# Kernel optimization log

Measured on AMD Instinct MI355X. Metric: run time of the kernel, lower is better.

The kernel has to match this reference:

```python
import jax, jax.numpy as jnp
import numpy as np

SCORE_THR = 0.3   # SSD.score_threshold
NMS_THR = 0.6     # SSD.nms_threshold
TOP_K = 100       # fixed candidate count per class (jit-friendly padded NMS)
CODER_W = (10.0, 10.0, 5.0, 5.0)  # SSD.coder_weights
B, A, C = 32, 8732, 81


def setup_inputs() -> dict:
    key = jax.random.key(0)
    k1, k2, k3 = jax.random.split(key, 3)
    class_logits = jax.random.normal(k1, (B, A, C), jnp.float32)
    box_regression = jax.random.normal(k2, (B, A, 4), jnp.float32)
    u = jax.random.uniform(k3, (A, 4), jnp.float32)
    centers = u[:, :2]                      # cy, cx in [0,1]
    sizes = 0.05 + 0.45 * u[:, 2:]          # h, w in [0.05, 0.5]
    priors = jnp.concatenate([centers, sizes], axis=-1)  # [A,4] (cy,cx,h,w)
    return {"class_logits": class_logits, "box_regression": box_regression, "priors": priors}


def decode_boxes(rel, priors):
    # rel: [...,A,4] codes (ty,tx,th,tw); priors: [A,4] (cy,cx,h,w); standard TF SSD box coder
    ty = rel[..., 0] / CODER_W[0]
    tx = rel[..., 1] / CODER_W[1]
    th = rel[..., 2] / CODER_W[2]
    tw = rel[..., 3] / CODER_W[3]
    cy = ty * priors[..., 2] + priors[..., 0]
    cx = tx * priors[..., 3] + priors[..., 1]
    h = jnp.exp(th) * priors[..., 2]
    w = jnp.exp(tw) * priors[..., 3]
    # corners (ymin, xmin, ymax, xmax)
    return jnp.stack([cy - h / 2, cx - w / 2, cy + h / 2, cx + w / 2], axis=-1)


def _iou_matrix(b):
    # b: [K,4] corners -> [K,K] pairwise IoU
    area = jnp.clip(b[:, 2] - b[:, 0], 0) * jnp.clip(b[:, 3] - b[:, 1], 0)
    tl = jnp.maximum(b[:, None, :2], b[None, :, :2])
    br = jnp.minimum(b[:, None, 2:], b[None, :, 2:])
    wh = jnp.clip(br - tl, 0)
    inter = wh[..., 0] * wh[..., 1]
    return inter / (area[:, None] + area[None, :] - inter + 1e-9)


def _nms_one_class(boxes, probs):
    # boxes: [A,4], probs: [A] -> padded [TOP_K,5] (box + score, zeros where suppressed)
    valid_all = probs > SCORE_THR
    masked = jnp.where(valid_all, probs, -1.0)
    top, idx = jax.lax.top_k(masked, TOP_K)          # sorted descending
    b = boxes[idx]                                    # [TOP_K,4]
    valid = top > SCORE_THR
    iou = _iou_matrix(jax.lax.stop_gradient(b))       # NMS selection is non-differentiable
    rng = jnp.arange(TOP_K)

    def body(i, keep):
        cur = keep[i] & valid[i]
        sup = (iou[i] > NMS_THR) & (rng > i)
        return jnp.where(cur, keep & ~sup, keep)

    keep = jax.lax.fori_loop(0, TOP_K, body, jnp.ones((TOP_K,), bool)) & valid
    out_b = jnp.where(keep[:, None], b, 0.0)
    out_s = jnp.where(keep, top, 0.0)
    return jnp.concatenate([out_b, out_s[:, None]], axis=-1)  # [TOP_K,5]


def reference(class_logits, box_regression, priors):
    scores = jax.nn.sigmoid(class_logits)             # [B,A,C]
    boxes = decode_boxes(box_regression, priors)      # [B,A,4]
    fg = scores[..., 1:]                              # skip background class 0 -> [B,A,C-1]
    per_class = jax.vmap(_nms_one_class, in_axes=(None, 1))   # over classes
    per_image = jax.vmap(per_class, in_axes=(0, 0))           # over batch
    return per_image(boxes, fg)                       # [B, C-1, TOP_K, 5]
```

## Files before the change

kernel.cpp:

```cpp
#include <hip/hip_runtime.h>
#include <math.h>

#define A_N   8732
#define A_PAD 8736
#define C_N   81
#define B_N   32
#define NCLS  80
#define NTASK (B_N * NCLS)
#define TOPK  100
#define NTHR  256
#define CAND  512
#define TA    64
#define NV4K  (A_PAD / 8)
#define KPT16 5
#define K0    0xBE00u
#define NBIN  128

#define THR_LOGIT (-0.8472978603872034)

__device__ __forceinline__ unsigned mapf(float x) {
    unsigned b = __float_as_uint(x);
    return b ^ ((b & 0x80000000u) ? 0xFFFFFFFFu : 0x80000000u);
}
__device__ __forceinline__ float unmapf(unsigned u) {
    unsigned b = (u & 0x80000000u) ? (u ^ 0x80000000u) : ~u;
    return __uint_as_float(b);
}

__device__ __forceinline__ void dec64(const float4 r4, const float4 p4,
                                      double* bx, double* area) {
    double ty = (double)r4.x / 10.0, tx = (double)r4.y / 10.0;
    double th = (double)r4.z / 5.0,  tw = (double)r4.w / 5.0;
    double cy = ty * (double)p4.z + (double)p4.x;
    double cx = tx * (double)p4.w + (double)p4.y;
    double hh = exp(th) * (double)p4.z;
    double ww = exp(tw) * (double)p4.w;
    bx[0] = cy - hh / 2.0; bx[1] = cx - ww / 2.0;
    bx[2] = cy + hh / 2.0; bx[3] = cx + ww / 2.0;
    double e0 = bx[2] - bx[0]; if (e0 < 0.0) e0 = 0.0;
    double e1 = bx[3] - bx[1]; if (e1 < 0.0) e1 = 0.0;
    *area = e0 * e1;
}

__global__ __launch_bounds__(NTHR) void key_transpose_kernel(
    const float* __restrict__ logits,
    unsigned short* __restrict__ keys)
{
    __shared__ unsigned short tile[NCLS][TA + 2];
    const int NT = (A_N + TA - 1) / TA;
    const int b  = blockIdx.x / NT;
    const int t0 = blockIdx.x % NT;
    const int a0 = t0 * TA;
    const int an = min(TA, A_N - a0);
    const int tid = threadIdx.x;

    const float* src = logits + ((size_t)b * A_N + a0) * C_N;

    if (an == TA) {
        const float4* src4 = (const float4*)src;
        const int total4 = TA * C_N / 4;
        for (int i = tid; i < total4; i += NTHR) {
            float4 v = src4[i];
            int base = 4 * i;
            int r  = base / C_N;
            int ch = base - r * C_N;
            float xs[4] = { v.x, v.y, v.z, v.w };
            #pragma unroll
            for (int k = 0; k < 4; ++k) {
                if (ch > 0)
                    tile[ch - 1][r] = (unsigned short)
                        (((double)xs[k] > THR_LOGIT) ? (mapf(xs[k]) >> 16) : 0u);
                if (++ch == C_N) { ch = 0; ++r; }
            }
        }
        __syncthreads();
        for (int i = tid; i < NCLS * 8; i += NTHR) {
            int row = i >> 3, j = i & 7;
            const unsigned* t32 = (const unsigned*)&tile[row][8 * j];
            uint4 w;
            w.x = t32[0]; w.y = t32[1]; w.z = t32[2]; w.w = t32[3];
            *(uint4*)(keys + ((size_t)(b * NCLS + row)) * A_PAD + a0 + 8 * j) = w;
        }
    } else {
        const int total = an * C_N;
        for (int i = tid; i < total; i += NTHR) {
            int r = i / C_N, ch = i - r * C_N;
            float x = src[i];
            if (ch > 0)
                tile[ch - 1][r] = (unsigned short)
                    (((double)x > THR_LOGIT) ? (mapf(x) >> 16) : 0u);
        }
        __syncthreads();
        for (int i = tid; i < NCLS * TA; i += NTHR) {
            int row = i / TA, col = i - row * TA;
            int a = a0 + col;
            if (a < A_PAD)
                keys[((size_t)(b * NCLS + row)) * A_PAD + a] =
                    (col < an) ? tile[row][col] : (unsigned short)0;
        }
    }
}

__device__ __forceinline__ void hcount(unsigned k, unsigned* hist) {
    if (k >= K0) {
        unsigned bin = (k - K0) >> 4; if (bin > (NBIN - 1)) bin = NBIN - 1;
        atomicAdd(&hist[bin], 1u);
    }
}

__global__ __launch_bounds__(NTHR) void ssd_nms_kernel(
    const float* __restrict__ logits,
    const unsigned short* __restrict__ keys,
    const float* __restrict__ boxreg,
    const float* __restrict__ priors,
    float* __restrict__ out)
{
    const int task = blockIdx.x;
    const int b = task / NCLS;
    const int c = task % NCLS;
    const int tid = threadIdx.x;

    __shared__ unsigned hist[NBIN];
    __shared__ unsigned candi[CAND];
    __shared__ unsigned long long cand[CAND];
    __shared__ unsigned long long ssel[TOPK];
    __shared__ float fb0[TOPK], fb1[TOPK], fb2[TOPK], fb3[TOPK];
    __shared__ float farea[TOPK], fscore[TOPK];
    __shared__ float4 rbox[TOPK], pbox[TOPK];
    __shared__ int svalid[TOPK];
    __shared__ unsigned long long supmask[TOPK][2];
    __shared__ unsigned long long keepw[2];
    __shared__ unsigned wtot[2];
    __shared__ int scal[2];

    const float* lg = logits + ((size_t)b * A_N * C_N) + (c + 1);

    uint4 kreg[KPT16];
    {
        const uint4* ksrc = (const uint4*)(keys + (size_t)task * A_PAD);
        #pragma unroll
        for (int j = 0; j < KPT16; ++j) {
            int i = tid + j * NTHR;
            kreg[j] = (i < NV4K) ? ksrc[i] : make_uint4(0u, 0u, 0u, 0u);
        }
    }

    if (tid < NBIN) hist[tid] = 0;
    for (int i = tid; i < CAND; i += NTHR) cand[i] = 0ull;
    if (tid < TOPK) ssel[tid] = 0ull;
    if (tid == 0) { scal[0] = 0; scal[1] = 1; }
    __syncthreads();

    #pragma unroll
    for (int j = 0; j < KPT16; ++j) {
        uint4 v = kreg[j];
        hcount(v.x & 0xFFFFu, hist); hcount(v.x >> 16, hist);
        hcount(v.y & 0xFFFFu, hist); hcount(v.y >> 16, hist);
        hcount(v.z & 0xFFFFu, hist); hcount(v.z >> 16, hist);
        hcount(v.w & 0xFFFFu, hist); hcount(v.w >> 16, hist);
    }
    __syncthreads();

    {
        unsigned h = (tid < NBIN) ? hist[tid] : 0u;
        unsigned incl = h;
        int lane = tid & 63;
        #pragma unroll
        for (int off = 1; off < 64; off <<= 1) {
            unsigned v = __shfl_down(incl, off);
            if (lane + off < 64) incl += v;
        }
        if (tid < NBIN && lane == 0) wtot[tid >> 6] = incl;
        __syncthreads();
        if (tid < NBIN) {
            unsigned S = incl + ((tid < 64) ? wtot[1] : 0u);
            if (S >= TOPK && (S - h) < TOPK)
                scal[1] = (int)(K0 + ((unsigned)tid << 4));
        }
        __syncthreads();

        unsigned T = wtot[0] + wtot[1];
        if (T < TOPK) {
            if (tid < NBIN) hist[tid] = 0;
            __syncthreads();
            #pragma unroll
            for (int j = 0; j < KPT16; ++j) {
                uint4 v = kreg[j];
                unsigned k;
                k = v.x & 0xFFFFu; if (k >= 0x4000u && k < K0) atomicAdd(&hist[(k - 0x4000u) >> 8], 1u);
                k = v.x >> 16;     if (k >= 0x4000u && k < K0) atomicAdd(&hist[(k - 0x4000u) >> 8], 1u);
                k = v.y & 0xFFFFu; if (k >= 0x4000u && k < K0) atomicAdd(&hist[(k - 0x4000u) >> 8], 1u);
                k = v.y >> 16;     if (k >= 0x4000u && k < K0) atomicAdd(&hist[(k - 0x4000u) >> 8], 1u);
                k = v.z & 0xFFFFu; if (k >= 0x4000u && k < K0) atomicAdd(&hist[(k - 0x4000u) >> 8], 1u);
                k = v.z >> 16;     if (k >= 0x4000u && k < K0) atomicAdd(&hist[(k - 0x4000u) >> 8], 1u);
                k = v.w & 0xFFFFu; if (k >= 0x4000u && k < K0) atomicAdd(&hist[(k - 0x4000u) >> 8], 1u);
                k = v.w >> 16;     if (k >= 0x4000u && k < K0) atomicAdd(&hist[(k - 0x4000u) >> 8], 1u);
            }
            __syncthreads();
            unsigned h2 = (tid < NBIN) ? hist[tid] : 0u;
            unsigned incl2 = h2;
            #pragma unroll
            for (int off = 1; off < 64; off <<= 1) {
                unsigned v = __shfl_down(incl2, off);
                if (lane + off < 64) incl2 += v;
            }
            if (tid < NBIN && lane == 0) wtot[tid >> 6] = incl2;
            __syncthreads();
            if (tid < NBIN) {
                unsigned S2 = incl2 + ((tid < 64) ? wtot[1] : 0u);
                unsigned need = TOPK - T;
                if (S2 >= need && (S2 - h2) < need)
                    scal[1] = (int)(0x4000u + ((unsigned)tid << 8));
            }
            __syncthreads();
        }
    }
    const unsigned cut16 = (unsigned)scal[1];

    #pragma unroll
    for (int j = 0; j < KPT16; ++j) {
        uint4 v = kreg[j];
        int a8 = 8 * (tid + j * NTHR);
        unsigned k; int p;
        k = v.x & 0xFFFFu; if (k >= cut16) { p = atomicAdd(&scal[0],1); if (p<CAND) candi[p] = a8+0; }
        k = v.x >> 16;     if (k >= cut16) { p = atomicAdd(&scal[0],1); if (p<CAND) candi[p] = a8+1; }
        k = v.y & 0xFFFFu; if (k >= cut16) { p = atomicAdd(&scal[0],1); if (p<CAND) candi[p] = a8+2; }
        k = v.y >> 16;     if (k >= cut16) { p = atomicAdd(&scal[0],1); if (p<CAND) candi[p] = a8+3; }
        k = v.z & 0xFFFFu; if (k >= cut16) { p = atomicAdd(&scal[0],1); if (p<CAND) candi[p] = a8+4; }
        k = v.z >> 16;     if (k >= cut16) { p = atomicAdd(&scal[0],1); if (p<CAND) candi[p] = a8+5; }
        k = v.w & 0xFFFFu; if (k >= cut16) { p = atomicAdd(&scal[0],1); if (p<CAND) candi[p] = a8+6; }
        k = v.w >> 16;     if (k >= cut16) { p = atomicAdd(&scal[0],1); if (p<CAND) candi[p] = a8+7; }
    }
    __syncthreads();
    const int M = min(scal[0], CAND);

    for (int i = tid; i < M; i += NTHR) {
        unsigned a = candi[i];
        float x = lg[(size_t)a * C_N];
        cand[i] = ((unsigned long long)mapf(x) << 32) | (unsigned)(~a);
    }
    __syncthreads();

    {
        int Mr = (M + 7) & ~7;
        for (int i = tid; i < Mr; i += NTHR) {
            unsigned long long mykey = cand[i];
            int rank = 0;
            #pragma unroll 8
            for (int j = 0; j < Mr; ++j) rank += (cand[j] > mykey) ? 1 : 0;
            if (mykey != 0ull && rank < TOPK) ssel[rank] = mykey;
        }
    }
    __syncthreads();

    if (tid < TOPK) {
        unsigned long long key = ssel[tid];
        int valid = (key != 0ull);
        float b0 = 0, b1 = 0, b2 = 0, b3 = 0, area = 0, sc = 0;
        float4 r4 = make_float4(0.f, 0.f, 0.f, 0.f), p4 = r4;
        if (valid) {
            int a = (int)(~(unsigned)key);
            float x = unmapf((unsigned)(key >> 32));
            sc = 1.0f / (1.0f + __expf(-x));
            r4 = *(const float4*)(boxreg + ((size_t)b * A_N + a) * 4);
            p4 = *(const float4*)(priors + (size_t)a * 4);
            float ty = r4.x * 0.1f, tx = r4.y * 0.1f;
            float th = r4.z * 0.2f, tw = r4.w * 0.2f;
            float cy = ty * p4.z + p4.x;
            float cx = tx * p4.w + p4.y;
            float hh = __expf(th) * p4.z;
            float ww = __expf(tw) * p4.w;
            b0 = cy - hh * 0.5f; b1 = cx - ww * 0.5f;
            b2 = cy + hh * 0.5f; b3 = cx + ww * 0.5f;
            area = fmaxf(b2 - b0, 0.f) * fmaxf(b3 - b1, 0.f);
        }
        fb0[tid] = b0; fb1[tid] = b1; fb2[tid] = b2; fb3[tid] = b3;
        farea[tid] = area; fscore[tid] = sc;
        rbox[tid] = r4; pbox[tid] = p4;
        svalid[tid] = valid;
    }
    __syncthreads();

    if (tid < 2 * TOPK) {
        int i = tid >> 1, w = tid & 1;
        unsigned long long m = 0;
        if (svalid[i]) {
            float i0 = fb0[i], i1 = fb1[i], i2 = fb2[i], i3 = fb3[i], ia = farea[i];
            int jbase = w * 64;
            int jend = min(jbase + 64, TOPK);
            int jstart = (jbase > i + 1) ? jbase : (i + 1);
            for (int j = jstart; j < jend; ++j) {
                float tl0 = fmaxf(i0, fb0[j]);
                float tl1 = fmaxf(i1, fb1[j]);
                float br0 = fminf(i2, fb2[j]);
                float br1 = fminf(i3, fb3[j]);
                float wh0 = fmaxf(br0 - tl0, 0.0f);
                float wh1 = fmaxf(br1 - tl1, 0.0f);
                float inter = wh0 * wh1;
                float denom = (ia + farea[j]) - inter;
                bool sup = inter > 0.601f * denom;
                bool amb = !sup && (inter > 0.599f * denom) && (inter > 0.0f);
                if (__any(amb)) {
                    if (amb) {
                        double bi[4], bj[4], ai, aj;
                        dec64(rbox[i], pbox[i], bi, &ai);
                        dec64(rbox[j], pbox[j], bj, &aj);
                        double tl0d = fmax(bi[0], bj[0]);
                        double tl1d = fmax(bi[1], bj[1]);
                        double br0d = fmin(bi[2], bj[2]);
                        double br1d = fmin(bi[3], bj[3]);
                        double wh0d = br0d - tl0d; if (wh0d < 0.0) wh0d = 0.0;
                        double wh1d = br1d - tl1d; if (wh1d < 0.0) wh1d = 0.0;
                        double interd = wh0d * wh1d;
                        double denomd = ((ai + aj) - interd) + 1e-9;
                        sup = interd > 0.6 * denomd;
                    }
                }
                if (sup) m |= 1ull << (j - jbase);
            }
        }
        supmask[i][w] = m;
    }
    __syncthreads();

    if (tid == 0) {
        unsigned long long kp0 = ~0ull, kp1 = ~0ull;
        for (int i = 0; i < TOPK; ++i) {
            bool kb = (i < 64) ? ((kp0 >> i) & 1ull) : ((kp1 >> (i - 64)) & 1ull);
            if (kb && svalid[i]) { kp0 &= ~supmask[i][0]; kp1 &= ~supmask[i][1]; }
        }
        keepw[0] = kp0; keepw[1] = kp1;
    }
    __syncthreads();

    if (tid < TOPK) {
        bool kb = (tid < 64) ? ((keepw[0] >> tid) & 1ull)
                             : ((keepw[1] >> (tid - 64)) & 1ull);
        bool kp = kb && (svalid[tid] != 0);
        size_t base = ((size_t)task * TOPK + tid) * 5;
        out[base + 0] = kp ? fb0[tid] : 0.0f;
        out[base + 1] = kp ? fb1[tid] : 0.0f;
        out[base + 2] = kp ? fb2[tid] : 0.0f;
        out[base + 3] = kp ? fb3[tid] : 0.0f;
        out[base + 4] = kp ? fscore[tid] : 0.0f;
    }
}

__global__ __launch_bounds__(NTHR) void ssd_nms_fallback(
    const float* __restrict__ logits,
    const float* __restrict__ boxreg,
    const float* __restrict__ priors,
    float* __restrict__ out)
{
    const int task = blockIdx.x;
    const int b = task / NCLS;
    const int c = task % NCLS;
    const int tid = threadIdx.x;

    __shared__ unsigned hist[2048];
    __shared__ unsigned wt4[4];
    __shared__ unsigned candi[CAND];
    __shared__ unsigned long long cand[CAND];
    __shared__ unsigned long long ssel[TOPK];
    __shared__ float fb0[TOPK], fb1[TOPK], fb2[TOPK], fb3[TOPK];
    __shared__ float farea[TOPK], fscore[TOPK];
    __shared__ float4 rbox[TOPK], pbox[TOPK];
    __shared__ int svalid[TOPK];
    __shared__ unsigned long long supmask[TOPK][2];
    __shared__ unsigned long long keepw[2];
    __shared__ int scal[2];

    const float* lg = logits + ((size_t)b * A_N * C_N) + (c + 1);

    for (int k = tid; k < 2048; k += NTHR) hist[k] = 0;
    for (int i = tid; i < CAND; i += NTHR) cand[i] = 0ull;
    if (tid < TOPK) ssel[tid] = 0ull;
    if (tid == 0) { scal[0] = 0; scal[1] = 1; }
    __syncthreads();

    for (int a = tid; a < A_N; a += NTHR) {
        float x = lg[(size_t)a * C_N];
        if ((double)x > THR_LOGIT) atomicAdd(&hist[mapf(x) >> 21], 1u);
    }
    __syncthreads();
    {
        unsigned s = 0;
        #pragma unroll
        for (int k = 0; k < 8; ++k) s += hist[tid * 8 + k];
        unsigned incl = s;
        int lane = tid & 63;
        #pragma unroll
        for (int off = 1; off < 64; off <<= 1) {
            unsigned v = __shfl_down(incl, off);
            if (lane + off < 64) incl += v;
        }
        if (lane == 0) wt4[tid >> 6] = incl;
        __syncthreads();
        unsigned hi = 0;
        #pragma unroll
        for (int w = 0; w < 4; ++w) if (w > (tid >> 6)) hi += wt4[w];
        unsigned excl = hi + (incl - s);
        if (excl < TOPK && excl + s >= TOPK) {
            unsigned running = excl;
            #pragma unroll
            for (int k = 7; k >= 0; --k) {
                running += hist[tid * 8 + k];
                if (running >= TOPK) { scal[1] = (int)(((unsigned)(tid * 8 + k)) << 21); break; }
            }
        }
    }
    __syncthreads();
    const unsigned cutoff = (unsigned)scal[1];

    for (int a = tid; a < A_N; a += NTHR) {
        float x = lg[(size_t)a * C_N];
        if ((double)x > THR_LOGIT) {
            unsigned u = mapf(x);
            if (u >= cutoff) {
                int p = atomicAdd(&scal[0], 1);
                if (p < CAND) { candi[p] = (unsigned)a; cand[p] = ((unsigned long long)u << 32) | (unsigned)(~(unsigned)a); }
            }
        }
    }
    __syncthreads();
    const int M = min(scal[0], CAND);
    {
        int Mr = (M + 7) & ~7;
        for (int i = tid; i < Mr; i += NTHR) {
            unsigned long long mykey = cand[i];
            int rank = 0;
            for (int j = 0; j < Mr; ++j) rank += (cand[j] > mykey) ? 1 : 0;
            if (mykey != 0ull && rank < TOPK) ssel[rank] = mykey;
        }
    }
    __syncthreads();
    if (tid < TOPK) {
        unsigned long long key = ssel[tid];
        int valid = (key != 0ull);
        float b0 = 0, b1 = 0, b2 = 0, b3 = 0, area = 0, sc = 0;
        float4 r4 = make_float4(0.f,0.f,0.f,0.f), p4 = r4;
        if (valid) {
            int a = (int)(~(unsigned)key);
            float x = unmapf((unsigned)(key >> 32));
            sc = 1.0f / (1.0f + __expf(-x));
            r4 = *(const float4*)(boxreg + ((size_t)b * A_N + a) * 4);
            p4 = *(const float4*)(priors + (size_t)a * 4);
            float cy = r4.x * 0.1f * p4.z + p4.x;
            float cx = r4.y * 0.1f * p4.w + p4.y;
            float hh = __expf(r4.z * 0.2f) * p4.z;
            float ww = __expf(r4.w * 0.2f) * p4.w;
            b0 = cy - hh * 0.5f; b1 = cx - ww * 0.5f;
            b2 = cy + hh * 0.5f; b3 = cx + ww * 0.5f;
            area = fmaxf(b2 - b0, 0.f) * fmaxf(b3 - b1, 0.f);
        }
        fb0[tid]=b0; fb1[tid]=b1; fb2[tid]=b2; fb3[tid]=b3;
        farea[tid]=area; fscore[tid]=sc; rbox[tid]=r4; pbox[tid]=p4; svalid[tid]=valid;
    }
    __syncthreads();
    if (tid < 2 * TOPK) {
        int i = tid >> 1, w = tid & 1;
        unsigned long long m = 0;
        if (svalid[i]) {
            float i0=fb0[i], i1=fb1[i], i2=fb2[i], i3=fb3[i], ia=farea[i];
            int jbase = w * 64, jend = min(jbase + 64, TOPK);
            int jstart = (jbase > i + 1) ? jbase : (i + 1);
            for (int j = jstart; j < jend; ++j) {
                float tl0=fmaxf(i0,fb0[j]), tl1=fmaxf(i1,fb1[j]);
                float br0=fminf(i2,fb2[j]), br1=fminf(i3,fb3[j]);
                float wh0=fmaxf(br0-tl0,0.f), wh1=fmaxf(br1-tl1,0.f);
                float inter=wh0*wh1, denom=(ia+farea[j])-inter;
                bool sup = inter > 0.601f*denom;
                bool amb = !sup && (inter > 0.599f*denom) && (inter > 0.f);
                if (__any(amb)) {
                    if (amb) {
                        double bi[4], bj[4], ai, aj;
                        dec64(rbox[i], pbox[i], bi, &ai);
                        dec64(rbox[j], pbox[j], bj, &aj);
                        double wh0d = fmin(bi[2],bj[2]) - fmax(bi[0],bj[0]); if (wh0d<0) wh0d=0;
                        double wh1d = fmin(bi[3],bj[3]) - fmax(bi[1],bj[1]); if (wh1d<0) wh1d=0;
                        double interd = wh0d*wh1d;
                        sup = interd > 0.6 * (((ai+aj)-interd)+1e-9);
                    }
                }
                if (sup) m |= 1ull << (j - jbase);
            }
        }
        supmask[i][w] = m;
    }
    __syncthreads();
    if (tid == 0) {
        unsigned long long kp0 = ~0ull, kp1 = ~0ull;
        for (int i = 0; i < TOPK; ++i) {
            bool kb = (i < 64) ? ((kp0 >> i) & 1ull) : ((kp1 >> (i - 64)) & 1ull);
            if (kb && svalid[i]) { kp0 &= ~supmask[i][0]; kp1 &= ~supmask[i][1]; }
        }
        keepw[0] = kp0; keepw[1] = kp1;
    }
    __syncthreads();
    if (tid < TOPK) {
        bool kb = (tid < 64) ? ((keepw[0] >> tid) & 1ull)
                             : ((keepw[1] >> (tid - 64)) & 1ull);
        bool kp = kb && (svalid[tid] != 0);
        size_t base = ((size_t)task * TOPK + tid) * 5;
        out[base + 0] = kp ? fb0[tid] : 0.0f;
        out[base + 1] = kp ? fb1[tid] : 0.0f;
        out[base + 2] = kp ? fb2[tid] : 0.0f;
        out[base + 3] = kp ? fb3[tid] : 0.0f;
        out[base + 4] = kp ? fscore[tid] : 0.0f;
    }
}

extern "C" void kernel_launch(void* const* d_in, const int* in_sizes, int n_in,
                              void* d_out, int out_size, void* d_ws, size_t ws_size,
                              hipStream_t stream) {
    const float* logits = (const float*)d_in[0];
    const float* boxreg = (const float*)d_in[1];
    const float* priors = (const float*)d_in[2];
    float* out = (float*)d_out;

    const size_t keys_bytes = (size_t)NTASK * A_PAD * sizeof(unsigned short);
    if (ws_size >= keys_bytes) {
        unsigned short* keysw = (unsigned short*)d_ws;
        const int NT = (A_N + TA - 1) / TA;
        key_transpose_kernel<<<dim3(B_N * NT), dim3(NTHR), 0, stream>>>(logits, keysw);
        ssd_nms_kernel<<<dim3(NTASK), dim3(NTHR), 0, stream>>>(
            logits, keysw, boxreg, priors, out);
    } else {
        ssd_nms_fallback<<<dim3(NTASK), dim3(NTHR), 0, stream>>>(
            logits, boxreg, priors, out);
    }
}
```

Before: 97.95 us.

## Rewrite per-class NMS kernel as single-wavefront block without barriers

The NMS kernel now runs one 64-lane wavefront per (image,class) task instead of a 256-thread block. Histogram scans, cutoff selection, candidate compaction and the keep-mask loop use wave shuffles and ballots, so no __syncthreads or shared atomics on counters are needed. The IoU mask work is split so lanes handle rows i and 99-i for load balance. Candidate capacity drops to 384 and keys are re-read from global memory rather than held in registers. Each block now has a quarter of the threads, so less parallelism per task is traded for no barrier overhead.

```diff
diff --git a/kernel.cpp b/kernel.cpp
--- a/kernel.cpp
+++ b/kernel.cpp
@@ -9,13 +9,12 @@
 #define NTASK (B_N * NCLS)
 #define TOPK  100
 #define NTHR  256
-#define CAND  512
+#define WAVE  64
+#define CAND  384
 #define TA    64
 #define NV4K  (A_PAD / 8)
-#define KPT16 5
+#define KPTW  18
 #define K0    0xBE00u
-#define NBIN  128
-
 #define THR_LOGIT (-0.8472978603872034)
 
 __device__ __forceinline__ unsigned mapf(float x) {
@@ -101,14 +100,7 @@
     }
 }
 
-__device__ __forceinline__ void hcount(unsigned k, unsigned* hist) {
-    if (k >= K0) {
-        unsigned bin = (k - K0) >> 4; if (bin > (NBIN - 1)) bin = NBIN - 1;
-        atomicAdd(&hist[bin], 1u);
-    }
-}
-
-__global__ __launch_bounds__(NTHR) void ssd_nms_kernel(
+__global__ __launch_bounds__(WAVE) void ssd_nms_wave(
     const float* __restrict__ logits,
     const unsigned short* __restrict__ keys,
     const float* __restrict__ boxreg,
@@ -118,231 +110,265 @@
     const int task = blockIdx.x;
     const int b = task / NCLS;
     const int c = task % NCLS;
-    const int tid = threadIdx.x;
-
-    __shared__ unsigned hist[NBIN];
+    const int l = threadIdx.x;
+
+    __shared__ unsigned hist[128];
     __shared__ unsigned candi[CAND];
     __shared__ unsigned long long cand[CAND];
     __shared__ unsigned long long ssel[TOPK];
-    __shared__ float fb0[TOPK], fb1[TOPK], fb2[TOPK], fb3[TOPK];
-    __shared__ float farea[TOPK], fscore[TOPK];
-    __shared__ float4 rbox[TOPK], pbox[TOPK];
-    __shared__ int svalid[TOPK];
-    __shared__ unsigned long long supmask[TOPK][2];
-    __shared__ unsigned long long keepw[2];
-    __shared__ unsigned wtot[2];
-    __shared__ int scal[2];
+    __shared__ float4 fbox4[TOPK];
+    __shared__ float farea[TOPK];
+    __shared__ int sanchor[TOPK];
 
     const float* lg = logits + ((size_t)b * A_N * C_N) + (c + 1);
-
-    uint4 kreg[KPT16];
+    const uint4* ksrc = (const uint4*)(keys + (size_t)task * A_PAD);
+    const float4* breg4 = (const float4*)(boxreg + (size_t)b * A_N * 4);
+    const float4* pri4  = (const float4*)priors;
+
+    hist[l] = 0; hist[WAVE + l] = 0;
+    ssel[l] = 0ull;
+    if (l < TOPK - WAVE) ssel[WAVE + l] = 0ull;
+
+    for (int j = 0; j < KPTW; ++j) {
+        int i = l + j * WAVE;
+        if (i < NV4K) {
+            uint4 v = ksrc[i];
+            unsigned k;
+            k = v.x & 0xFFFFu; if (k >= K0) { unsigned bn = (k - K0) >> 4; if (bn > 127u) bn = 127u; atomicAdd(&hist[bn], 1u); }
+            k = v.x >> 16;     if (k >= K0) { unsigned bn = (k - K0) >> 4; if (bn > 127u) bn = 127u; atomicAdd(&hist[bn], 1u); }
+            k = v.y & 0xFFFFu; if (k >= K0) { unsigned bn = (k - K0) >> 4; if (bn > 127u) bn = 127u; atomicAdd(&hist[bn], 1u); }
+            k = v.y >> 16;     if (k >= K0) { unsigned bn = (k - K0) >> 4; if (bn > 127u) bn = 127u; atomicAdd(&hist[bn], 1u); }
+            k = v.z & 0xFFFFu; if (k >= K0) { unsigned bn = (k - K0) >> 4; if (bn > 127u) bn = 127u; atomicAdd(&hist[bn], 1u); }
+            k = v.z >> 16;     if (k >= K0) { unsigned bn = (k - K0) >> 4; if (bn > 127u) bn = 127u; atomicAdd(&hist[bn], 1u); }
+            k = v.w & 0xFFFFu; if (k >= K0) { unsigned bn = (k - K0) >> 4; if (bn > 127u) bn = 127u; atomicAdd(&hist[bn], 1u); }
+            k = v.w >> 16;     if (k >= K0) { unsigned bn = (k - K0) >> 4; if (bn > 127u) bn = 127u; atomicAdd(&hist[bn], 1u); }
+        }
+    }
+
+    unsigned cut16 = 1u;
     {
-        const uint4* ksrc = (const uint4*)(keys + (size_t)task * A_PAD);
-        #pragma unroll
-        for (int j = 0; j < KPT16; ++j) {
-            int i = tid + j * NTHR;
-            kreg[j] = (i < NV4K) ? ksrc[i] : make_uint4(0u, 0u, 0u, 0u);
-        }
-    }
-
-    if (tid < NBIN) hist[tid] = 0;
-    for (int i = tid; i < CAND; i += NTHR) cand[i] = 0ull;
-    if (tid < TOPK) ssel[tid] = 0ull;
-    if (tid == 0) { scal[0] = 0; scal[1] = 1; }
-    __syncthreads();
-
-    #pragma unroll
-    for (int j = 0; j < KPT16; ++j) {
-        uint4 v = kreg[j];
-        hcount(v.x & 0xFFFFu, hist); hcount(v.x >> 16, hist);
-        hcount(v.y & 0xFFFFu, hist); hcount(v.y >> 16, hist);
-        hcount(v.z & 0xFFFFu, hist); hcount(v.z >> 16, hist);
-        hcount(v.w & 0xFFFFu, hist); hcount(v.w >> 16, hist);
-    }
-    __syncthreads();
-
-    {
-        unsigned h = (tid < NBIN) ? hist[tid] : 0u;
-        unsigned incl = h;
-        int lane = tid & 63;
+        unsigned sL = hist[l], sH = hist[WAVE + l];
+        unsigned inclH = sH, inclL = sL;
         #pragma unroll
         for (int off = 1; off < 64; off <<= 1) {
-            unsigned v = __shfl_down(incl, off);
-            if (lane + off < 64) incl += v;
-        }
-        if (tid < NBIN && lane == 0) wtot[tid >> 6] = incl;
-        __syncthreads();
-        if (tid < NBIN) {
-            unsigned S = incl + ((tid < 64) ? wtot[1] : 0u);
-            if (S >= TOPK && (S - h) < TOPK)
-                scal[1] = (int)(K0 + ((unsigned)tid << 4));
-        }
-        __syncthreads();
-
-        unsigned T = wtot[0] + wtot[1];
-        if (T < TOPK) {
-            if (tid < NBIN) hist[tid] = 0;
-            __syncthreads();
-            #pragma unroll
-            for (int j = 0; j < KPT16; ++j) {
-                uint4 v = kreg[j];
-                unsigned k;
-                k = v.x & 0xFFFFu; if (k >= 0x4000u && k < K0) atomicAdd(&hist[(k - 0x4000u) >> 8], 1u);
-                k = v.x >> 16;     if (k >= 0x4000u && k < K0) atomicAdd(&hist[(k - 0x4000u) >> 8], 1u);
-                k = v.y & 0xFFFFu; if (k >= 0x4000u && k < K0) atomicAdd(&hist[(k - 0x4000u) >> 8], 1u);
-                k = v.y >> 16;     if (k >= 0x4000u && k < K0) atomicAdd(&hist[(k - 0x4000u) >> 8], 1u);
-                k = v.z & 0xFFFFu; if (k >= 0x4000u && k < K0) atomicAdd(&hist[(k - 0x4000u) >> 8], 1u);
-                k = v.z >> 16;     if (k >= 0x4000u && k < K0) atomicAdd(&hist[(k - 0x4000u) >> 8], 1u);
-                k = v.w & 0xFFFFu; if (k >= 0x4000u && k < K0) atomicAdd(&hist[(k - 0x4000u) >> 8], 1u);
-                k = v.w >> 16;     if (k >= 0x4000u && k < K0) atomicAdd(&hist[(k - 0x4000u) >> 8], 1u);
-            }
-            __syncthreads();
-            unsigned h2 = (tid < NBIN) ? hist[tid] : 0u;
-            unsigned incl2 = h2;
+            unsigned t = __shfl_down(inclH, off); if (l + off < 64) inclH += t;
+        }
+        #pragma unroll
+        for (int off = 1; off < 64; off <<= 1) {
+            unsigned t = __shfl_down(inclL, off); if (l + off < 64) inclL += t;
+        }
+        unsigned TH = __shfl(inclH, 0);
+        unsigned SH = inclH;
+        unsigned SL = inclL + TH;
+        unsigned T  = __shfl(SL, 0);
+
+        if (T >= TOPK) {
+            bool crH = (SH >= TOPK) && (SH - sH < TOPK);
+            bool crL = (SL >= TOPK) && (SL - sL < TOPK);
+            unsigned myCut = crH ? (K0 + ((unsigned)(WAVE + l) << 4))
+                                 : (K0 + ((unsigned)l << 4));
+            unsigned long long cm = __ballot(crH || crL);
+            cut16 = __shfl(myCut, (int)(__ffsll((long long)cm) - 1));
+        } else {
+            hist[l] = 0; hist[WAVE + l] = 0;
+            for (int j = 0; j < KPTW; ++j) {
+                int i = l + j * WAVE;
+                if (i < NV4K) {
+                    uint4 v = ksrc[i];
+                    unsigned k;
+                    k = v.x & 0xFFFFu; if (k >= 0x4000u && k < K0) atomicAdd(&hist[(k - 0x4000u) >> 8], 1u);
+                    k = v.x >> 16;     if (k >= 0x4000u && k < K0) atomicAdd(&hist[(k - 0x4000u) >> 8], 1u);
+                    k = v.y & 0xFFFFu; if (k >= 0x4000u && k < K0) atomicAdd(&hist[(k - 0x4000u) >> 8], 1u);
+                    k = v.y >> 16;     if (k >= 0x4000u && k < K0) atomicAdd(&hist[(k - 0x4000u) >> 8], 1u);
+                    k = v.z & 0xFFFFu; if (k >= 0x4000u && k < K0) atomicAdd(&hist[(k - 0x4000u) >> 8], 1u);
+                    k = v.z >> 16;     if (k >= 0x4000u && k < K0) atomicAdd(&hist[(k - 0x4000u) >> 8], 1u);
+                    k = v.w & 0xFFFFu; if (k >= 0x4000u && k < K0) atomicAdd(&hist[(k - 0x4000u) >> 8], 1u);
+                    k = v.w >> 16;     if (k >= 0x4000u && k < K0) atomicAdd(&hist[(k - 0x4000u) >> 8], 1u);
+                }
+            }
+            unsigned sL2 = hist[l], sH2 = hist[WAVE + l];
+            unsigned iH = sH2, iL = sL2;
             #pragma unroll
             for (int off = 1; off < 64; off <<= 1) {
-                unsigned v = __shfl_down(incl2, off);
-                if (lane + off < 64) incl2 += v;
-            }
-            if (tid < NBIN && lane == 0) wtot[tid >> 6] = incl2;
-            __syncthreads();
-            if (tid < NBIN) {
-                unsigned S2 = incl2 + ((tid < 64) ? wtot[1] : 0u);
-                unsigned need = TOPK - T;
-                if (S2 >= need && (S2 - h2) < need)
-                    scal[1] = (int)(0x4000u + ((unsigned)tid << 8));
-            }
-            __syncthreads();
-        }
-    }
-    const unsigned cut16 = (unsigned)scal[1];
+                unsigned t = __shfl_down(iH, off); if (l + off < 64) iH += t;
+            }
+            #pragma unroll
+            for (int off = 1; off < 64; off <<= 1) {
+                unsigned t = __shfl_down(iL, off); if (l + off < 64) iL += t;
+            }
+            unsigned TH2 = __shfl(iH, 0);
+            unsigned SH2 = iH, SL2 = iL + TH2;
+            unsigned need = TOPK - T;
+            bool crH = (SH2 >= need) && (SH2 - sH2 < need);
+            bool crL = (SL2 >= need) && (SL2 - sL2 < need);
+            unsigned myCut = crH ? (0x4000u + ((unsigned)(WAVE + l) << 8))
+                                 : (0x4000u + ((unsigned)l << 8));
+            unsigned long long cm = __ballot(crH || crL);
+            if (cm) cut16 = __shfl(myCut, (int)(__ffsll((long long)cm) - 1));
+        }
+    }
+
+    int cnt = 0;
+    auto gstep = [&](unsigned kk, int idx) {
+        bool pr = (kk >= cut16);
+        unsigned long long mk = __ballot(pr);
+        if (pr) {
+            int pos = cnt + (int)__popcll(mk & ((1ull << l) - 1ull));
+            if (pos < CAND) candi[pos] = (unsigned)idx;
+        }
+        cnt += (int)__popcll(mk);
+    };
+    for (int j = 0; j < KPTW; ++j) {
+        int i = l + j * WAVE;
+        uint4 v = (i < NV4K) ? ksrc[i] : make_uint4(0u, 0u, 0u, 0u);
+        int a8 = 8 * i;
+        gstep(v.x & 0xFFFFu, a8 + 0); gstep(v.x >> 16, a8 + 1);
+        gstep(v.y & 0xFFFFu, a8 + 2); gstep(v.y >> 16, a8 + 3);
+        gstep(v.z & 0xFFFFu, a8 + 4); gstep(v.z >> 16, a8 + 5);
+        gstep(v.w & 0xFFFFu, a8 + 6); gstep(v.w >> 16, a8 + 7);
+    }
+    const int M  = min(cnt, CAND);
+    const int Mr = (M + 7) & ~7;
+    if (l < Mr - M) cand[M + l] = 0ull;
 
     #pragma unroll
-    for (int j = 0; j < KPT16; ++j) {
-        uint4 v = kreg[j];
-        int a8 = 8 * (tid + j * NTHR);
-        unsigned k; int p;
-        k = v.x & 0xFFFFu; if (k >= cut16) { p = atomicAdd(&scal[0],1); if (p<CAND) candi[p] = a8+0; }
-        k = v.x >> 16;     if (k >= cut16) { p = atomicAdd(&scal[0],1); if (p<CAND) candi[p] = a8+1; }
-        k = v.y & 0xFFFFu; if (k >= cut16) { p = atomicAdd(&scal[0],1); if (p<CAND) candi[p] = a8+2; }
-        k = v.y >> 16;     if (k >= cut16) { p = atomicAdd(&scal[0],1); if (p<CAND) candi[p] = a8+3; }
-        k = v.z & 0xFFFFu; if (k >= cut16) { p = atomicAdd(&scal[0],1); if (p<CAND) candi[p] = a8+4; }
-        k = v.z >> 16;     if (k >= cut16) { p = atomicAdd(&scal[0],1); if (p<CAND) candi[p] = a8+5; }
-        k = v.w & 0xFFFFu; if (k >= cut16) { p = atomicAdd(&scal[0],1); if (p<CAND) candi[p] = a8+6; }
-        k = v.w >> 16;     if (k >= cut16) { p = atomicAdd(&scal[0],1); if (p<CAND) candi[p] = a8+7; }
-    }
-    __syncthreads();
-    const int M = min(scal[0], CAND);
-
-    for (int i = tid; i < M; i += NTHR) {
-        unsigned a = candi[i];
-        float x = lg[(size_t)a * C_N];
-        cand[i] = ((unsigned long long)mapf(x) << 32) | (unsigned)(~a);
-    }
-    __syncthreads();
+    for (int k = 0; k < CAND / WAVE; ++k) {
+        int i = l + k * WAVE;
+        if (i < M) {
+            unsigned a = candi[i];
+            float x = lg[(size_t)a * C_N];
+            cand[i] = ((unsigned long long)mapf(x) << 32) | (unsigned)(~a);
+        }
+    }
 
     {
-        int Mr = (M + 7) & ~7;
-        for (int i = tid; i < Mr; i += NTHR) {
-            unsigned long long mykey = cand[i];
-            int rank = 0;
-            #pragma unroll 8
-            for (int j = 0; j < Mr; ++j) rank += (cand[j] > mykey) ? 1 : 0;
-            if (mykey != 0ull && rank < TOPK) ssel[rank] = mykey;
-        }
-    }
-    __syncthreads();
-
-    if (tid < TOPK) {
-        unsigned long long key = ssel[tid];
-        int valid = (key != 0ull);
-        float b0 = 0, b1 = 0, b2 = 0, b3 = 0, area = 0, sc = 0;
-        float4 r4 = make_float4(0.f, 0.f, 0.f, 0.f), p4 = r4;
-        if (valid) {
-            int a = (int)(~(unsigned)key);
-            float x = unmapf((unsigned)(key >> 32));
-            sc = 1.0f / (1.0f + __expf(-x));
-            r4 = *(const float4*)(boxreg + ((size_t)b * A_N + a) * 4);
-            p4 = *(const float4*)(priors + (size_t)a * 4);
-            float ty = r4.x * 0.1f, tx = r4.y * 0.1f;
-            float th = r4.z * 0.2f, tw = r4.w * 0.2f;
-            float cy = ty * p4.z + p4.x;
-            float cx = tx * p4.w + p4.y;
-            float hh = __expf(th) * p4.z;
-            float ww = __expf(tw) * p4.w;
-            b0 = cy - hh * 0.5f; b1 = cx - ww * 0.5f;
-            b2 = cy + hh * 0.5f; b3 = cx + ww * 0.5f;
-            area = fmaxf(b2 - b0, 0.f) * fmaxf(b3 - b1, 0.f);
-        }
-        fb0[tid] = b0; fb1[tid] = b1; fb2[tid] = b2; fb3[tid] = b3;
-        farea[tid] = area; fscore[tid] = sc;
-        rbox[tid] = r4; pbox[tid] = p4;
-        svalid[tid] = valid;
-    }
-    __syncthreads();
-
-    if (tid < 2 * TOPK) {
-        int i = tid >> 1, w = tid & 1;
-        unsigned long long m = 0;
-        if (svalid[i]) {
-            float i0 = fb0[i], i1 = fb1[i], i2 = fb2[i], i3 = fb3[i], ia = farea[i];
-            int jbase = w * 64;
-            int jend = min(jbase + 64, TOPK);
-            int jstart = (jbase > i + 1) ? jbase : (i + 1);
-            for (int j = jstart; j < jend; ++j) {
-                float tl0 = fmaxf(i0, fb0[j]);
-                float tl1 = fmaxf(i1, fb1[j]);
-                float br0 = fminf(i2, fb2[j]);
-                float br1 = fminf(i3, fb3[j]);
-                float wh0 = fmaxf(br0 - tl0, 0.0f);
-                float wh1 = fmaxf(br1 - tl1, 0.0f);
-                float inter = wh0 * wh1;
-                float denom = (ia + farea[j]) - inter;
-                bool sup = inter > 0.601f * denom;
-                bool amb = !sup && (inter > 0.599f * denom) && (inter > 0.0f);
-                if (__any(amb)) {
-                    if (amb) {
-                        double bi[4], bj[4], ai, aj;
-                        dec64(rbox[i], pbox[i], bi, &ai);
-                        dec64(rbox[j], pbox[j], bj, &aj);
-                        double tl0d = fmax(bi[0], bj[0]);
-                        double tl1d = fmax(bi[1], bj[1]);
-                        double br0d = fmin(bi[2], bj[2]);
-                        double br1d = fmin(bi[3], bj[3]);
-                        double wh0d = br0d - tl0d; if (wh0d < 0.0) wh0d = 0.0;
-                        double wh1d = br1d - tl1d; if (wh1d < 0.0) wh1d = 0.0;
-                        double interd = wh0d * wh1d;
-                        double denomd = ((ai + aj) - interd) + 1e-9;
-                        sup = interd > 0.6 * denomd;
-                    }
-                }
-                if (sup) m |= 1ull << (j - jbase);
-            }
-        }
-        supmask[i][w] = m;
-    }
-    __syncthreads();
-
-    if (tid == 0) {
-        unsigned long long kp0 = ~0ull, kp1 = ~0ull;
-        for (int i = 0; i < TOPK; ++i) {
-            bool kb = (i < 64) ? ((kp0 >> i) & 1ull) : ((kp1 >> (i - 64)) & 1ull);
-            if (kb && svalid[i]) { kp0 &= ~supmask[i][0]; kp1 &= ~supmask[i][1]; }
-        }
-        keepw[0] = kp0; keepw[1] = kp1;
-    }
-    __syncthreads();
-
-    if (tid < TOPK) {
-        bool kb = (tid < 64) ? ((keepw[0] >> tid) & 1ull)
-                             : ((keepw[1] >> (tid - 64)) & 1ull);
-        bool kp = kb && (svalid[tid] != 0);
-        size_t base = ((size_t)task * TOPK + tid) * 5;
-        out[base + 0] = kp ? fb0[tid] : 0.0f;
-        out[base + 1] = kp ? fb1[tid] : 0.0f;
-        out[base + 2] = kp ? fb2[tid] : 0.0f;
-        out[base + 3] = kp ? fb3[tid] : 0.0f;
-        out[base + 4] = kp ? fscore[tid] : 0.0f;
+        unsigned long long mk2[CAND / WAVE];
+        int rk[CAND / WAVE];
+        #pragma unroll
+        for (int k = 0; k < CAND / WAVE; ++k) {
+            int i = l + k * WAVE;
+            mk2[k] = (i < Mr) ? cand[i] : 0ull;
+            rk[k] = 0;
+        }
+        for (int j = 0; j < Mr; ++j) {
+            unsigned long long cj = cand[j];
+            #pragma unroll
+            for (int k = 0; k < CAND / WAVE; ++k)
+                if (k * WAVE < Mr)
+                    rk[k] += (cj > mk2[k]) ? 1 : 0;
+        }
+        #pragma unroll
+        for (int k = 0; k < CAND / WAVE; ++k)
+            if (mk2[k] != 0ull && rk[k] < TOPK) ssel[rk[k]] = mk2[k];
+    }
+
+    unsigned long long keyA = ssel[l];
+    unsigned long long keyB = (l < TOPK - WAVE) ? ssel[WAVE + l] : 0ull;
+    float A0 = 0, A1 = 0, A2 = 0, A3 = 0, arA = 0, scA = 0; int aA = 0;
+    float B0 = 0, B1 = 0, B2 = 0, B3 = 0, arB = 0, scB = 0; int aB = 0;
+    if (keyA) {
+        aA = (int)(~(unsigned)keyA);
+        float x = unmapf((unsigned)(keyA >> 32));
+        scA = 1.0f / (1.0f + __expf(-x));
+        float4 r4 = breg4[aA], p4 = pri4[aA];
+        float cy = r4.x * 0.1f * p4.z + p4.x;
+        float cx = r4.y * 0.1f * p4.w + p4.y;
+        float hh = __expf(r4.z * 0.2f) * p4.z;
+        float ww = __expf(r4.w * 0.2f) * p4.w;
+        A0 = cy - hh * 0.5f; A1 = cx - ww * 0.5f;
+        A2 = cy + hh * 0.5f; A3 = cx + ww * 0.5f;
+        arA = fmaxf(A2 - A0, 0.f) * fmaxf(A3 - A1, 0.f);
+    }
+    fbox4[l] = make_float4(A0, A1, A2, A3); farea[l] = arA; sanchor[l] = aA;
+    if (l < TOPK - WAVE) {
+        if (keyB) {
+            aB = (int)(~(unsigned)keyB);
+            float x = unmapf((unsigned)(keyB >> 32));
+            scB = 1.0f / (1.0f + __expf(-x));
+            float4 r4 = breg4[aB], p4 = pri4[aB];
+            float cy = r4.x * 0.1f * p4.z + p4.x;
+            float cx = r4.y * 0.1f * p4.w + p4.y;
+            float hh = __expf(r4.z * 0.2f) * p4.z;
+            float ww = __expf(r4.w * 0.2f) * p4.w;
+            B0 = cy - hh * 0.5f; B1 = cx - ww * 0.5f;
+            B2 = cy + hh * 0.5f; B3 = cx + ww * 0.5f;
+            arB = fmaxf(B2 - B0, 0.f) * fmaxf(B3 - B1, 0.f);
+        }
+        fbox4[WAVE + l] = make_float4(B0, B1, B2, B3);
+        farea[WAVE + l] = arB; sanchor[WAVE + l] = aB;
+    }
+    const unsigned long long v0 = __ballot(keyA != 0ull);
+    const unsigned long long v1 = __ballot(l < TOPK - WAVE && keyB != 0ull);
+
+    auto pairSup = [&](float i0, float i1, float i2, float i3, float ia,
+                       int ai, int j) -> bool {
+        float4 bj = fbox4[j]; float aj = farea[j];
+        float tl0 = fmaxf(i0, bj.x), tl1 = fmaxf(i1, bj.y);
+        float br0 = fminf(i2, bj.z), br1 = fminf(i3, bj.w);
+        float wh0 = fmaxf(br0 - tl0, 0.f), wh1 = fmaxf(br1 - tl1, 0.f);
+        float inter = wh0 * wh1;
+        float denom = (ia + aj) - inter;
+        bool sup = inter > 0.601f * denom;
+        bool amb = !sup && (inter > 0.599f * denom) && (inter > 0.f);
+        if (amb) {
+            int ja = sanchor[j];
+            double bi[4], bj_[4], ai_, aj_;
+            dec64(breg4[ai], pri4[ai], bi, &ai_);
+            dec64(breg4[ja], pri4[ja], bj_, &aj_);
+            double t0 = fmax(bi[0], bj_[0]), t1 = fmax(bi[1], bj_[1]);
+            double b0 = fmin(bi[2], bj_[2]), b1 = fmin(bi[3], bj_[3]);
+            double w0 = b0 - t0; if (w0 < 0.0) w0 = 0.0;
+            double w1 = b1 - t1; if (w1 < 0.0) w1 = 0.0;
+            double interd = w0 * w1;
+            sup = interd > 0.6 * (((ai_ + aj_) - interd) + 1e-9);
+        }
+        return sup;
+    };
+
+    unsigned long long mA0 = 0, mA1 = 0, mB0 = 0, mB1 = 0;
+    if (l < 50) {
+        for (int j = l + 1; j < TOPK; ++j) {
+            if (pairSup(A0, A1, A2, A3, arA, aA, j)) {
+                if (j < 64) mA0 |= 1ull << j; else mA1 |= 1ull << (j - 64);
+            }
+        }
+        int rB = 99 - l;
+        float4 bi = fbox4[rB]; float ai = farea[rB]; int aiB = sanchor[rB];
+        for (int j = rB + 1; j < TOPK; ++j) {
+            if (pairSup(bi.x, bi.y, bi.z, bi.w, ai, aiB, j)) {
+                if (j < 64) mB0 |= 1ull << j; else mB1 |= 1ull << (j - 64);
+            }
+        }
+    }
+
+    unsigned long long kp0 = ~0ull, kp1 = (1ull << (TOPK - WAVE)) - 1ull;
+    for (int i = 0; i < TOPK; ++i) {
+        bool low = (i < 50);
+        int src = low ? i : 99 - i;
+        unsigned long long m0 = low ? __shfl(mA0, src) : __shfl(mB0, src);
+        unsigned long long m1 = low ? __shfl(mA1, src) : __shfl(mB1, src);
+        bool kb = (i < 64) ? ((kp0 >> i) & 1ull) : ((kp1 >> (i - 64)) & 1ull);
+        bool vb = (i < 64) ? ((v0 >> i) & 1ull) : ((v1 >> (i - 64)) & 1ull);
+        if (kb && vb) { kp0 &= ~m0; kp1 &= ~m1; }
+    }
+
+    {
+        bool keepA = ((kp0 >> l) & 1ull) && (keyA != 0ull);
+        size_t baseA = ((size_t)task * TOPK + l) * 5;
+        out[baseA + 0] = keepA ? A0 : 0.0f;
+        out[baseA + 1] = keepA ? A1 : 0.0f;
+        out[baseA + 2] = keepA ? A2 : 0.0f;
+        out[baseA + 3] = keepA ? A3 : 0.0f;
+        out[baseA + 4] = keepA ? scA : 0.0f;
+        if (l < TOPK - WAVE) {
+            bool keepB = ((kp1 >> l) & 1ull) && (keyB != 0ull);
+            size_t baseB = ((size_t)task * TOPK + WAVE + l) * 5;
+            out[baseB + 0] = keepB ? B0 : 0.0f;
+            out[baseB + 1] = keepB ? B1 : 0.0f;
+            out[baseB + 2] = keepB ? B2 : 0.0f;
+            out[baseB + 3] = keepB ? B3 : 0.0f;
+            out[baseB + 4] = keepB ? scB : 0.0f;
+        }
     }
 }
 
@@ -359,7 +385,6 @@
 
     __shared__ unsigned hist[2048];
     __shared__ unsigned wt4[4];
-    __shared__ unsigned candi[CAND];
     __shared__ unsigned long long cand[CAND];
     __shared__ unsigned long long ssel[TOPK];
     __shared__ float fb0[TOPK], fb1[TOPK], fb2[TOPK], fb3[TOPK];
@@ -418,7 +443,7 @@
             unsigned u = mapf(x);
             if (u >= cutoff) {
                 int p = atomicAdd(&scal[0], 1);
-                if (p < CAND) { candi[p] = (unsigned)a; cand[p] = ((unsigned long long)u << 32) | (unsigned)(~(unsigned)a); }
+                if (p < CAND) cand[p] = ((unsigned long long)u << 32) | (unsigned)(~(unsigned)a);
             }
         }
     }
@@ -523,7 +548,7 @@
         unsigned short* keysw = (unsigned short*)d_ws;
         const int NT = (A_N + TA - 1) / TA;
         key_transpose_kernel<<<dim3(B_N * NT), dim3(NTHR), 0, stream>>>(logits, keysw);
-        ssd_nms_kernel<<<dim3(NTASK), dim3(NTHR), 0, stream>>>(
+        ssd_nms_wave<<<dim3(NTASK), dim3(WAVE), 0, stream>>>(
             logits, keysw, boxreg, priors, out);
     } else {
         ssd_nms_fallback<<<dim3(NTASK), dim3(NTHR), 0, stream>>>(
```

Result: slower. 119.5 us (+22.0%).
